# Kernel tuning notes

Hardware: AMD Instinct MI355X
Metric: run time of the kernel (lower is better)

## Reference

```python
import jax, jax.numpy as jnp
import numpy as np

N_NODES = 100_000
N_EDGES = 3_200_000
NUM_FEATURES = 128
EMB = 128
GNN_LAYERS = 3
N_GRAPHS = 512
FILL = 2.0  # improved=True -> self-loop weight 2


def setup_inputs() -> dict:
    key = jax.random.key(0)
    ks = jax.random.split(key, 8)
    x = jax.random.normal(ks[0], (N_NODES, NUM_FEATURES), jnp.float32)
    edge_index = jax.random.randint(ks[1], (2, N_EDGES), 0, N_NODES, dtype=jnp.int64)
    batch_index = jnp.sort(jax.random.randint(ks[2], (N_NODES,), 0, N_GRAPHS, dtype=jnp.int64))
    W0 = jax.random.normal(ks[3], (NUM_FEATURES, EMB), jnp.float32) / np.float32(np.sqrt(NUM_FEATURES))
    b0 = jnp.zeros((EMB,), jnp.float32)
    W_hid = jax.random.normal(ks[4], (GNN_LAYERS - 1, EMB, EMB), jnp.float32) / np.float32(np.sqrt(EMB))
    b_hid = jnp.zeros((GNN_LAYERS - 1, EMB), jnp.float32)
    W_out = jax.random.normal(ks[5], (2 * EMB, 1), jnp.float32) / np.float32(np.sqrt(2 * EMB))
    b_out = jnp.zeros((1,), jnp.float32)
    return {"x": x, "edge_index": edge_index, "batch_index": batch_index,
            "W0": W0, "b0": b0, "W_hid": W_hid, "b_hid": b_hid,
            "W_out": W_out, "b_out": b_out}


def _gcn_norm(edge_index, n_nodes):
    # add self-loops (weight=FILL for improved=True), symmetric D^-1/2 A D^-1/2 norm
    loop = jnp.arange(n_nodes)
    row = jnp.concatenate([edge_index[0], loop])
    col = jnp.concatenate([edge_index[1], loop])
    w = jnp.concatenate([jnp.ones((edge_index.shape[1],), jnp.float32),
                         jnp.full((n_nodes,), FILL, jnp.float32)])
    deg = jax.ops.segment_sum(w, col, num_segments=n_nodes)
    dinv = jnp.where(deg > 0, jax.lax.rsqrt(deg), 0.0)
    return row, col, dinv[row] * w * dinv[col]


def _gcn_conv(h, W, b, row, col, norm, n_nodes):
    h = h @ W                              # [N, emb]
    msg = h[row] * norm[:, None]           # gather + scale over edges
    return jax.ops.segment_sum(msg, col, num_segments=n_nodes) + b


def reference(x, edge_index, batch_index, W0, b0, W_hid, b_hid, W_out, b_out):
    n = x.shape[0]
    row, col, norm = _gcn_norm(edge_index, n)
    h = jnp.tanh(_gcn_conv(x, W0, b0, row, col, norm, n))
    for i in range(W_hid.shape[0]):
        h = jnp.tanh(_gcn_conv(h, W_hid[i], b_hid[i], row, col, norm, n))
    cnt = jax.ops.segment_sum(jnp.ones((n,), h.dtype), batch_index, num_segments=N_GRAPHS)
    mx = jax.ops.segment_max(h, batch_index, num_segments=N_GRAPHS)
    mx = jnp.where(cnt[:, None] > 0, mx, 0.0)            # gmp
    mean = jax.ops.segment_sum(h, batch_index, num_segments=N_GRAPHS) / jnp.maximum(cnt, 1.0)[:, None]  # gap
    pooled = jnp.concatenate([mx, mean], axis=1)          # [G, 2*emb]
    return pooled @ W_out + b_out                         # [G, 1]
```

## Files before the change

### kernel.cpp

```cpp
#include <hip/hip_runtime.h>
#include <math.h>

#define NF 128
#define SCAN_CHUNK 1024
#define BUCK_SHIFT 9
#define BUCK_CAP 20480
#define NBUCK_MAX 256
#define ECHUNK 2048

typedef int      vint4   __attribute__((ext_vector_type(4)));
typedef float    vfloat4 __attribute__((ext_vector_type(4)));
typedef float    f32x4   __attribute__((ext_vector_type(4)));
typedef _Float16 vhalf4  __attribute__((ext_vector_type(4)));
typedef _Float16 vhalf8  __attribute__((ext_vector_type(8)));

__global__ __launch_bounds__(256) void k_bucket(const int* __restrict__ row,
                                                const int* __restrict__ col,
                                                int* __restrict__ gcur,
                                                int* __restrict__ bdata, int E) {
  __shared__ int bcnt[NBUCK_MAX];
  __shared__ int bstage[NBUCK_MAX][32];
  const int tid = threadIdx.x;
  const int nChunks = (E + ECHUNK - 1) / ECHUNK;

  for (int chunk = blockIdx.x; chunk < nChunks; chunk += gridDim.x) {
    bcnt[tid] = 0;
    __syncthreads();

    const int cbase = chunk * ECHUNK;
    if (cbase + ECHUNK <= E) {
      const vint4* r4 = reinterpret_cast<const vint4*>(row) + (cbase >> 2) + 2 * tid;
      const vint4* c4 = reinterpret_cast<const vint4*>(col) + (cbase >> 2) + 2 * tid;
      vint4 ra = __builtin_nontemporal_load(&r4[0]);
      vint4 rb = __builtin_nontemporal_load(&r4[1]);
      vint4 ca = __builtin_nontemporal_load(&c4[0]);
      vint4 cb = __builtin_nontemporal_load(&c4[1]);
      int rr[8] = {ra.x, ra.y, ra.z, ra.w, rb.x, rb.y, rb.z, rb.w};
      int cc[8] = {ca.x, ca.y, ca.z, ca.w, cb.x, cb.y, cb.z, cb.w};
#pragma unroll
      for (int j = 0; j < 8; ++j) {
        int b = cc[j] >> BUCK_SHIFT;
        int packed = ((cc[j] & ((1 << BUCK_SHIFT) - 1)) << 17) | rr[j];
        int pos = atomicAdd(&bcnt[b], 1);
        if (pos < 32) {
          bstage[b][pos] = packed;
        } else {
          int p = atomicAdd(&gcur[b], 1);
          if (p < BUCK_CAP) bdata[b * BUCK_CAP + p] = packed;
        }
      }
    } else {
      for (int j = 0; j < 8; ++j) {
        int e = cbase + tid + j * 256;
        if (e < E) {
          int c = col[e], r = row[e];
          int b = c >> BUCK_SHIFT;
          int packed = ((c & ((1 << BUCK_SHIFT) - 1)) << 17) | r;
          int pos = atomicAdd(&bcnt[b], 1);
          if (pos < 32) {
            bstage[b][pos] = packed;
          } else {
            int p = atomicAdd(&gcur[b], 1);
            if (p < BUCK_CAP) bdata[b * BUCK_CAP + p] = packed;
          }
        }
      }
    }
    __syncthreads();

    int k = bcnt[tid];
    if (k > 32) k = 32;
    if (k > 0) {
      int p = atomicAdd(&gcur[tid], k);
      for (int i = 0; i < k && p + i < BUCK_CAP; ++i)
        bdata[tid * BUCK_CAP + p + i] = bstage[tid][i];
    }
    __syncthreads();
  }
}

__global__ __launch_bounds__(256) void k_hist(const int* __restrict__ gcur,
                                              const int* __restrict__ bdata,
                                              int* __restrict__ cnt, int N) {
  __shared__ int hist[1 << BUCK_SHIFT];
  const int b = blockIdx.x;
  const int tid = threadIdx.x;
  hist[tid] = 0;
  hist[tid + 256] = 0;
  __syncthreads();
  int nb = gcur[b];
  if (nb > BUCK_CAP) nb = BUCK_CAP;
  const int* bd = bdata + (size_t)b * BUCK_CAP;
  for (int i = tid; i < nb; i += 256) atomicAdd(&hist[bd[i] >> 17], 1);
  __syncthreads();
  int base = b << BUCK_SHIFT;
#pragma unroll
  for (int k = 0; k < (1 << BUCK_SHIFT); k += 256) {
    int node = base + k + tid;
    if (node < N) cnt[node] = hist[k + tid];
  }
}

__global__ __launch_bounds__(256) void k_scanA(const int* __restrict__ cnt,
                                               int* __restrict__ chunkTot, int N) {
  int c0 = blockIdx.x * SCAN_CHUNK + threadIdx.x * 4;
  int s = 0;
#pragma unroll
  for (int j = 0; j < 4; ++j) {
    int idx = c0 + j;
    if (idx < N) s += cnt[idx];
  }
  __shared__ int red[256];
  red[threadIdx.x] = s;
  __syncthreads();
  for (int o = 128; o > 0; o >>= 1) {
    if (threadIdx.x < o) red[threadIdx.x] += red[threadIdx.x + o];
    __syncthreads();
  }
  if (threadIdx.x == 0) chunkTot[blockIdx.x] = red[0];
}

__global__ __launch_bounds__(128) void k_scanB(const int* __restrict__ chunkTot,
                                               int* __restrict__ chunkOff, int nChunks) {
  __shared__ int buf[128];
  int t = threadIdx.x;
  int v = (t < nChunks) ? chunkTot[t] : 0;
  buf[t] = v;
  __syncthreads();
  for (int o = 1; o < 128; o <<= 1) {
    int x = buf[t];
    if (t >= o) x += buf[t - o];
    __syncthreads();
    buf[t] = x;
    __syncthreads();
  }
  if (t < nChunks) chunkOff[t] = buf[t] - v;
}

__global__ __launch_bounds__(256) void k_scanC(const int* __restrict__ cnt,
                                               const int* __restrict__ chunkOff,
                                               int* __restrict__ offs,
                                               float* __restrict__ dinv, int N) {
  int t = threadIdx.x;
  int c0 = blockIdx.x * SCAN_CHUNK + t * 4;
  int v[4];
  int s = 0;
#pragma unroll
  for (int j = 0; j < 4; ++j) {
    int idx = c0 + j;
    v[j] = (idx < N) ? cnt[idx] : 0;
    s += v[j];
  }
  __shared__ int buf[256];
  buf[t] = s;
  __syncthreads();
  for (int o = 1; o < 256; o <<= 1) {
    int x = buf[t];
    if (t >= o) x += buf[t - o];
    __syncthreads();
    buf[t] = x;
    __syncthreads();
  }
  int excl = buf[t] - s + chunkOff[blockIdx.x];
#pragma unroll
  for (int j = 0; j < 4; ++j) {
    int idx = c0 + j;
    if (idx < N) {
      offs[idx] = excl;
      dinv[idx] = rsqrtf((float)v[j] + 2.0f);
      excl += v[j];
    }
  }
}

__global__ __launch_bounds__(256) void k_bfill(const int* __restrict__ gcur,
                                               const int* __restrict__ bdata,
                                               const int* __restrict__ offs,
                                               int* __restrict__ csr, int N) {
  __shared__ int lcur[1 << BUCK_SHIFT];
  const int b = blockIdx.x;
  const int tid = threadIdx.x;
  const int base = b << BUCK_SHIFT;
#pragma unroll
  for (int k = 0; k < (1 << BUCK_SHIFT); k += 256) {
    int node = base + k + tid;
    lcur[k + tid] = (node < N) ? offs[node] : 0;
  }
  __syncthreads();
  int nb = gcur[b];
  if (nb > BUCK_CAP) nb = BUCK_CAP;
  const int* bd = bdata + (size_t)b * BUCK_CAP;
  for (int i = tid; i < nb; i += 256) {
    int v = bd[i];
    int p = atomicAdd(&lcur[v >> 17], 1);
    csr[p] = v & 0x1FFFF;
  }
}

__global__ __launch_bounds__(256) void k_wcvt(const float* __restrict__ W0,
                                              const float* __restrict__ Whid,
                                              _Float16* __restrict__ wt) {
  int g = blockIdx.x * 1024 + threadIdx.x * 4;
#pragma unroll
  for (int j = 0; j < 4; ++j) {
    int idx = g + j;
    int layer = idx >> 14;
    int within = idx & 16383;
    int c = within >> 7, k = within & 127;
    const float* src = (layer == 0) ? W0 : Whid + (layer - 1) * 16384;
    wt[idx] = (_Float16)src[k * 128 + c];
  }
}

template <bool F32IN>
__global__ __launch_bounds__(256) void k_gemm(const void* __restrict__ Hin,
                                              const _Float16* __restrict__ Wt,
                                              const float* __restrict__ dinv,
                                              _Float16* __restrict__ out, int nRows) {
  __shared__ _Float16 Wl[128][136];

  const int tid = threadIdx.x;
  for (int i = tid; i < 128 * 16; i += 256) {
    int r = i >> 4, seg = i & 15;
    *reinterpret_cast<vhalf8*>(&Wl[r][seg * 8]) =
        *reinterpret_cast<const vhalf8*>(Wt + r * 128 + seg * 8);
  }
  __syncthreads();

  const int l = tid & 63;
  const int wv = tid >> 6;
  const int lidx = l & 15;
  const int lk8 = (l >> 4) * 8;
  const int nodeBase = blockIdx.x * 128 + wv * 32;

  vhalf8 hfrag[2][4];
#pragma unroll
  for (int g = 0; g < 2; ++g) {
    int node = nodeBase + g * 16 + lidx;
    if (node < nRows) {
      if constexpr (F32IN) {
        const float* hp = (const float*)Hin + (size_t)node * NF + lk8;
#pragma unroll
        for (int kc = 0; kc < 4; ++kc) {
          vfloat4 lo = *reinterpret_cast<const vfloat4*>(hp + kc * 32);
          vfloat4 hi = *reinterpret_cast<const vfloat4*>(hp + kc * 32 + 4);
          vhalf8 v;
          v[0] = (_Float16)lo.x; v[1] = (_Float16)lo.y;
          v[2] = (_Float16)lo.z; v[3] = (_Float16)lo.w;
          v[4] = (_Float16)hi.x; v[5] = (_Float16)hi.y;
          v[6] = (_Float16)hi.z; v[7] = (_Float16)hi.w;
          hfrag[g][kc] = v;
        }
      } else {
        const _Float16* hp = (const _Float16*)Hin + (size_t)node * NF + lk8;
#pragma unroll
        for (int kc = 0; kc < 4; ++kc)
          hfrag[g][kc] = *reinterpret_cast<const vhalf8*>(hp + kc * 32);
      }
    } else {
#pragma unroll
      for (int kc = 0; kc < 4; ++kc)
#pragma unroll
        for (int j = 0; j < 8; ++j) hfrag[g][kc][j] = (_Float16)0.f;
    }
  }

  f32x4 acc[2][8];
#pragma unroll
  for (int g = 0; g < 2; ++g)
#pragma unroll
    for (int ct = 0; ct < 8; ++ct) acc[g][ct] = (f32x4)(0.f);

#pragma unroll
  for (int kc = 0; kc < 4; ++kc) {
#pragma unroll
    for (int ct = 0; ct < 8; ++ct) {
      vhalf8 w = *reinterpret_cast<const vhalf8*>(&Wl[ct * 16 + lidx][kc * 32 + lk8]);
      acc[0][ct] = __builtin_amdgcn_mfma_f32_16x16x32_f16(w, hfrag[0][kc], acc[0][ct], 0, 0, 0);
      acc[1][ct] = __builtin_amdgcn_mfma_f32_16x16x32_f16(w, hfrag[1][kc], acc[1][ct], 0, 0, 0);
    }
  }

  const int f0 = (l >> 4) * 4;
#pragma unroll
  for (int g = 0; g < 2; ++g) {
    int node = nodeBase + g * 16 + lidx;
    if (node < nRows) {
      float dv = dinv[node];
#pragma unroll
      for (int ct = 0; ct < 8; ++ct) {
        vhalf4 o;
        o.x = (_Float16)(dv * acc[g][ct][0]);
        o.y = (_Float16)(dv * acc[g][ct][1]);
        o.z = (_Float16)(dv * acc[g][ct][2]);
        o.w = (_Float16)(dv * acc[g][ct][3]);
        *reinterpret_cast<vhalf4*>(out + (size_t)node * NF + ct * 16 + f0) = o;
      }
    }
  }
}

__device__ __forceinline__ float4 h2f(vhalf4 v) {
  return make_float4((float)v.x, (float)v.y, (float)v.z, (float)v.w);
}
__device__ __forceinline__ float4 add4(float4 a, float4 acc) {
  acc.x += a.x; acc.y += a.y; acc.z += a.z; acc.w += a.w;
  return acc;
}

__global__ __launch_bounds__(256) void k_agg(const _Float16* __restrict__ tmp,
                                             const int* __restrict__ offs,
                                             const int* __restrict__ cnt,
                                             const int* __restrict__ csr,
                                             const float* __restrict__ dinv,
                                             const float* __restrict__ bias,
                                             _Float16* __restrict__ hout, int N) {
  int node = (blockIdx.x * 256 + threadIdx.x) >> 5;
  if (node >= N) return;
  int lane = threadIdx.x & 31;

  float dv = dinv[node];

  const vhalf4* t4 = reinterpret_cast<const vhalf4*>(tmp);
  float4 hv = h2f(t4[(size_t)node * 32 + lane]);
  float4 acc = make_float4(2.f * hv.x, 2.f * hv.y, 2.f * hv.z, 2.f * hv.w);

  int s = offs[node], e = s + cnt[node];
  int i = s;

  for (; (i & 3) && i < e; ++i) {
    float4 a = h2f(t4[(size_t)csr[i] * 32 + lane]);
    acc = add4(a, acc);
  }

  const vint4* cp = reinterpret_cast<const vint4*>(csr);
  for (; i + 8 <= e; i += 8) {
    vint4 p0 = __builtin_nontemporal_load(&cp[(i >> 2) + 0]);
    vint4 p1 = __builtin_nontemporal_load(&cp[(i >> 2) + 1]);
    float4 a0 = h2f(t4[(size_t)p0.x * 32 + lane]);
    float4 a1 = h2f(t4[(size_t)p0.y * 32 + lane]);
    float4 a2 = h2f(t4[(size_t)p0.z * 32 + lane]);
    float4 a3 = h2f(t4[(size_t)p0.w * 32 + lane]);
    float4 a4 = h2f(t4[(size_t)p1.x * 32 + lane]);
    float4 a5 = h2f(t4[(size_t)p1.y * 32 + lane]);
    float4 a6 = h2f(t4[(size_t)p1.z * 32 + lane]);
    float4 a7 = h2f(t4[(size_t)p1.w * 32 + lane]);
    acc = add4(a0, acc); acc = add4(a1, acc);
    acc = add4(a2, acc); acc = add4(a3, acc);
    acc = add4(a4, acc); acc = add4(a5, acc);
    acc = add4(a6, acc); acc = add4(a7, acc);
  }
  for (; i + 4 <= e; i += 4) {
    vint4 p = __builtin_nontemporal_load(&cp[i >> 2]);
    float4 a0 = h2f(t4[(size_t)p.x * 32 + lane]);
    float4 a1 = h2f(t4[(size_t)p.y * 32 + lane]);
    float4 a2 = h2f(t4[(size_t)p.z * 32 + lane]);
    float4 a3 = h2f(t4[(size_t)p.w * 32 + lane]);
    acc = add4(a0, acc); acc = add4(a1, acc);
    acc = add4(a2, acc); acc = add4(a3, acc);
  }
  for (; i < e; ++i) {
    float4 a = h2f(t4[(size_t)csr[i] * 32 + lane]);
    acc = add4(a, acc);
  }

  float4 b4 = reinterpret_cast<const float4*>(bias)[lane];
  vhalf4 r;
  r.x = (_Float16)tanhf(fmaf(dv, acc.x, b4.x));
  r.y = (_Float16)tanhf(fmaf(dv, acc.y, b4.y));
  r.z = (_Float16)tanhf(fmaf(dv, acc.z, b4.z));
  r.w = (_Float16)tanhf(fmaf(dv, acc.w, b4.w));
  __builtin_nontemporal_store(r, &reinterpret_cast<vhalf4*>(hout)[(size_t)node * 32 + lane]);
}

__global__ __launch_bounds__(512) void k_pool(const _Float16* __restrict__ h,
                                              const int* __restrict__ batch,
                                              const float* __restrict__ Wout,
                                              const float* __restrict__ bout,
                                              float* __restrict__ out, int N) {
  int g = blockIdx.x;

  int lo = 0, hi = N;
  while (lo < hi) { int mid = (lo + hi) >> 1; if (batch[mid] < g) lo = mid + 1; else hi = mid; }
  int s = lo;
  int lo2 = s, hi2 = N;
  while (lo2 < hi2) { int mid = (lo2 + hi2) >> 1; if (batch[mid] < g + 1) lo2 = mid + 1; else hi2 = mid; }
  int e = lo2;

  const int seg = threadIdx.x & 15;
  const int stripe = threadIdx.x >> 4;

  float mx[8], sm[8];
#pragma unroll
  for (int j = 0; j < 8; ++j) { mx[j] = -INFINITY; sm[j] = 0.f; }

  for (int n = s + stripe; n < e; n += 32) {
    vhalf8 v = *reinterpret_cast<const vhalf8*>(h + (size_t)n * NF + seg * 8);
#pragma unroll
    for (int j = 0; j < 8; ++j) {
      float f = (float)v[j];
      mx[j] = fmaxf(mx[j], f);
      sm[j] += f;
    }
  }

  __shared__ float smx[32][NF];
  __shared__ float ssm[32][NF];
#pragma unroll
  for (int j = 0; j < 8; ++j) {
    smx[stripe][seg * 8 + j] = mx[j];
    ssm[stripe][seg * 8 + j] = sm[j];
  }
  __syncthreads();

  for (int half = 16; half >= 1; half >>= 1) {
    if (stripe < half) {
#pragma unroll
      for (int j = 0; j < 8; ++j) {
        int f = seg * 8 + j;
        smx[stripe][f] = fmaxf(smx[stripe][f], smx[stripe + half][f]);
        ssm[stripe][f] += ssm[stripe + half][f];
      }
    }
    __syncthreads();
  }

  float part = 0.f;
  if (threadIdx.x < NF) {
    int f = threadIdx.x;
    float mxv = smx[0][f];
    float smv = ssm[0][f];
    int cntg = e - s;
    float mean = smv / fmaxf((float)cntg, 1.0f);
    if (cntg == 0) mxv = 0.f;
    part = mxv * Wout[f] + mean * Wout[NF + f];
  }
  for (int o = 32; o > 0; o >>= 1) part += __shfl_down(part, o);
  __shared__ float wsum[8];
  if ((threadIdx.x & 63) == 0) wsum[threadIdx.x >> 6] = part;
  __syncthreads();
  if (threadIdx.x == 0) out[g] = wsum[0] + wsum[1] + bout[0];
}

extern "C" void kernel_launch(void* const* d_in, const int* in_sizes, int n_in,
                              void* d_out, int out_size, void* d_ws, size_t ws_size,
                              hipStream_t stream) {
  const float* x     = (const float*)d_in[0];
  const int*   eidx  = (const int*)d_in[1];
  const int*   batch = (const int*)d_in[2];
  const float* W0    = (const float*)d_in[3];
  const float* b0    = (const float*)d_in[4];
  const float* Whid  = (const float*)d_in[5];
  const float* bhid  = (const float*)d_in[6];
  const float* Wout  = (const float*)d_in[7];
  const float* bout  = (const float*)d_in[8];
  float* out = (float*)d_out;

  const int N = in_sizes[0] / NF;
  const int E = in_sizes[1] / 2;
  const int G = out_size;

  const int* erow = eidx;
  const int* ecol = eidx + E;

  size_t off = 0;
  auto alloc = [&](size_t bytes) -> void* {
    void* p = (char*)d_ws + off;
    off += (bytes + 255) & ~(size_t)255;
    return p;
  };
  int*      gcur     = (int*)alloc(NBUCK_MAX * 4);
  int*      cnt      = (int*)alloc((size_t)N * 4);
  float*    dinv     = (float*)alloc((size_t)N * 4);
  int*      offs     = (int*)alloc((size_t)N * 4);
  int*      chunkTot = (int*)alloc(1024);
  int*      chunkOff = (int*)alloc(1024);
  int*      bdata    = (int*)alloc((size_t)NBUCK_MAX * BUCK_CAP * 4);
  int*      csr      = (int*)alloc((size_t)E * 4);
  _Float16* wt       = (_Float16*)alloc(3 * 16384 * 2);
  _Float16* tmp      = (_Float16*)alloc((size_t)N * NF * 2);
  _Float16* h        = (_Float16*)alloc((size_t)N * NF * 2);
  (void)ws_size;

  (void)hipMemsetAsync(gcur, 0, NBUCK_MAX * 4, stream);

  const int nChunks = (N + SCAN_CHUNK - 1) / SCAN_CHUNK;
  const int nbuck = (N + (1 << BUCK_SHIFT) - 1) >> BUCK_SHIFT;

  k_bucket<<<512, 256, 0, stream>>>(erow, ecol, gcur, bdata, E);
  k_hist<<<nbuck, 256, 0, stream>>>(gcur, bdata, cnt, N);
  k_scanA<<<nChunks, 256, 0, stream>>>(cnt, chunkTot, N);
  k_scanB<<<1, 128, 0, stream>>>(chunkTot, chunkOff, nChunks);
  k_scanC<<<nChunks, 256, 0, stream>>>(cnt, chunkOff, offs, dinv, N);
  k_bfill<<<nbuck, 256, 0, stream>>>(gcur, bdata, offs, csr, N);
  k_wcvt<<<48, 256, 0, stream>>>(W0, Whid, wt);

  const int gemmGrid = (N + 127) / 128;
  const int aggGrid = (N + 7) / 8;

  k_gemm<true><<<gemmGrid, 256, 0, stream>>>(x, wt, dinv, tmp, N);
  k_agg<<<aggGrid, 256, 0, stream>>>(tmp, offs, cnt, csr, dinv, b0, h, N);
  k_gemm<false><<<gemmGrid, 256, 0, stream>>>(h, wt + 16384, dinv, tmp, N);
  k_agg<<<aggGrid, 256, 0, stream>>>(tmp, offs, cnt, csr, dinv, bhid, h, N);
  k_gemm<false><<<gemmGrid, 256, 0, stream>>>(h, wt + 2 * 16384, dinv, tmp, N);
  k_agg<<<aggGrid, 256, 0, stream>>>(tmp, offs, cnt, csr, dinv, bhid + NF, h, N);

  k_pool<<<G, 512, 0, stream>>>(h, batch, Wout, bout, out, N);
}
```

Measured before the change: 520.1 us.

## Fuse histogram, scan and CSR fill into one per-bucket build kernel

Replaces the histogram, three-stage global prefix scan and bucket fill kernels with a single per-bucket kernel. Each bucket computes its own local histogram and scan, and writes CSR entries into a padded per-bucket region (offset b*BUCK_CAP), so no global scan is needed. This removes four kernel launches and a round trip of the count array through global memory. In exchange the CSR becomes sparse with gaps between buckets, using more memory and giving slightly less contiguous neighbour reads in aggregation.

```diff
diff --git a/kernel.cpp b/kernel.cpp
--- a/kernel.cpp
+++ b/kernel.cpp
@@ -2,7 +2,6 @@
 #include <math.h>
 
 #define NF 128
-#define SCAN_CHUNK 1024
 #define BUCK_SHIFT 9
 #define BUCK_CAP 20480
 #define NBUCK_MAX 256
@@ -79,117 +78,52 @@
   }
 }
 
-__global__ __launch_bounds__(256) void k_hist(const int* __restrict__ gcur,
-                                              const int* __restrict__ bdata,
-                                              int* __restrict__ cnt, int N) {
+__global__ __launch_bounds__(256) void k_build(const int* __restrict__ gcur,
+                                               const int* __restrict__ bdata,
+                                               int* __restrict__ csr,
+                                               int* __restrict__ offs,
+                                               int* __restrict__ cnt,
+                                               float* __restrict__ dinv, int N) {
   __shared__ int hist[1 << BUCK_SHIFT];
+  __shared__ int buf[256];
+  __shared__ int lcur[1 << BUCK_SHIFT];
   const int b = blockIdx.x;
   const int tid = threadIdx.x;
   hist[tid] = 0;
   hist[tid + 256] = 0;
   __syncthreads();
+
   int nb = gcur[b];
   if (nb > BUCK_CAP) nb = BUCK_CAP;
   const int* bd = bdata + (size_t)b * BUCK_CAP;
   for (int i = tid; i < nb; i += 256) atomicAdd(&hist[bd[i] >> 17], 1);
   __syncthreads();
-  int base = b << BUCK_SHIFT;
-#pragma unroll
-  for (int k = 0; k < (1 << BUCK_SHIFT); k += 256) {
-    int node = base + k + tid;
-    if (node < N) cnt[node] = hist[k + tid];
-  }
-}
-
-__global__ __launch_bounds__(256) void k_scanA(const int* __restrict__ cnt,
-                                               int* __restrict__ chunkTot, int N) {
-  int c0 = blockIdx.x * SCAN_CHUNK + threadIdx.x * 4;
-  int s = 0;
-#pragma unroll
-  for (int j = 0; j < 4; ++j) {
-    int idx = c0 + j;
-    if (idx < N) s += cnt[idx];
-  }
-  __shared__ int red[256];
-  red[threadIdx.x] = s;
-  __syncthreads();
-  for (int o = 128; o > 0; o >>= 1) {
-    if (threadIdx.x < o) red[threadIdx.x] += red[threadIdx.x + o];
-    __syncthreads();
-  }
-  if (threadIdx.x == 0) chunkTot[blockIdx.x] = red[0];
-}
-
-__global__ __launch_bounds__(128) void k_scanB(const int* __restrict__ chunkTot,
-                                               int* __restrict__ chunkOff, int nChunks) {
-  __shared__ int buf[128];
-  int t = threadIdx.x;
-  int v = (t < nChunks) ? chunkTot[t] : 0;
-  buf[t] = v;
-  __syncthreads();
-  for (int o = 1; o < 128; o <<= 1) {
-    int x = buf[t];
-    if (t >= o) x += buf[t - o];
-    __syncthreads();
-    buf[t] = x;
-    __syncthreads();
-  }
-  if (t < nChunks) chunkOff[t] = buf[t] - v;
-}
-
-__global__ __launch_bounds__(256) void k_scanC(const int* __restrict__ cnt,
-                                               const int* __restrict__ chunkOff,
-                                               int* __restrict__ offs,
-                                               float* __restrict__ dinv, int N) {
-  int t = threadIdx.x;
-  int c0 = blockIdx.x * SCAN_CHUNK + t * 4;
-  int v[4];
-  int s = 0;
-#pragma unroll
-  for (int j = 0; j < 4; ++j) {
-    int idx = c0 + j;
-    v[j] = (idx < N) ? cnt[idx] : 0;
-    s += v[j];
-  }
-  __shared__ int buf[256];
-  buf[t] = s;
+
+  int h0 = hist[2 * tid];
+  int h1 = hist[2 * tid + 1];
+  int s = h0 + h1;
+  buf[tid] = s;
   __syncthreads();
   for (int o = 1; o < 256; o <<= 1) {
-    int x = buf[t];
-    if (t >= o) x += buf[t - o];
-    __syncthreads();
-    buf[t] = x;
-    __syncthreads();
-  }
-  int excl = buf[t] - s + chunkOff[blockIdx.x];
-#pragma unroll
-  for (int j = 0; j < 4; ++j) {
-    int idx = c0 + j;
-    if (idx < N) {
-      offs[idx] = excl;
-      dinv[idx] = rsqrtf((float)v[j] + 2.0f);
-      excl += v[j];
-    }
-  }
-}
-
-__global__ __launch_bounds__(256) void k_bfill(const int* __restrict__ gcur,
-                                               const int* __restrict__ bdata,
-                                               const int* __restrict__ offs,
-                                               int* __restrict__ csr, int N) {
-  __shared__ int lcur[1 << BUCK_SHIFT];
-  const int b = blockIdx.x;
-  const int tid = threadIdx.x;
-  const int base = b << BUCK_SHIFT;
-#pragma unroll
-  for (int k = 0; k < (1 << BUCK_SHIFT); k += 256) {
-    int node = base + k + tid;
-    lcur[k + tid] = (node < N) ? offs[node] : 0;
-  }
-  __syncthreads();
-  int nb = gcur[b];
-  if (nb > BUCK_CAP) nb = BUCK_CAP;
-  const int* bd = bdata + (size_t)b * BUCK_CAP;
+    int x = buf[tid];
+    if (tid >= o) x += buf[tid - o];
+    __syncthreads();
+    buf[tid] = x;
+    __syncthreads();
+  }
+  int excl = buf[tid] - s;
+
+  const int nbase = b << BUCK_SHIFT;
+  const int cbase = b * BUCK_CAP;
+  int o0 = cbase + excl;
+  int o1 = o0 + h0;
+  lcur[2 * tid] = o0;
+  lcur[2 * tid + 1] = o1;
+  int n0 = nbase + 2 * tid, n1 = n0 + 1;
+  if (n0 < N) { offs[n0] = o0; cnt[n0] = h0; dinv[n0] = rsqrtf((float)h0 + 2.0f); }
+  if (n1 < N) { offs[n1] = o1; cnt[n1] = h1; dinv[n1] = rsqrtf((float)h1 + 2.0f); }
+  __syncthreads();
+
   for (int i = tid; i < nb; i += 256) {
     int v = bd[i];
     int p = atomicAdd(&lcur[v >> 17], 1);
@@ -473,10 +407,8 @@
   int*      cnt      = (int*)alloc((size_t)N * 4);
   float*    dinv     = (float*)alloc((size_t)N * 4);
   int*      offs     = (int*)alloc((size_t)N * 4);
-  int*      chunkTot = (int*)alloc(1024);
-  int*      chunkOff = (int*)alloc(1024);
   int*      bdata    = (int*)alloc((size_t)NBUCK_MAX * BUCK_CAP * 4);
-  int*      csr      = (int*)alloc((size_t)E * 4);
+  int*      csr      = (int*)alloc((size_t)NBUCK_MAX * BUCK_CAP * 4);
   _Float16* wt       = (_Float16*)alloc(3 * 16384 * 2);
   _Float16* tmp      = (_Float16*)alloc((size_t)N * NF * 2);
   _Float16* h        = (_Float16*)alloc((size_t)N * NF * 2);
@@ -484,15 +416,10 @@
 
   (void)hipMemsetAsync(gcur, 0, NBUCK_MAX * 4, stream);
 
-  const int nChunks = (N + SCAN_CHUNK - 1) / SCAN_CHUNK;
   const int nbuck = (N + (1 << BUCK_SHIFT) - 1) >> BUCK_SHIFT;
 
   k_bucket<<<512, 256, 0, stream>>>(erow, ecol, gcur, bdata, E);
-  k_hist<<<nbuck, 256, 0, stream>>>(gcur, bdata, cnt, N);
-  k_scanA<<<nChunks, 256, 0, stream>>>(cnt, chunkTot, N);
-  k_scanB<<<1, 128, 0, stream>>>(chunkTot, chunkOff, nChunks);
-  k_scanC<<<nChunks, 256, 0, stream>>>(cnt, chunkOff, offs, dinv, N);
-  k_bfill<<<nbuck, 256, 0, stream>>>(gcur, bdata, offs, csr, N);
+  k_build<<<nbuck, 256, 0, stream>>>(gcur, bdata, csr, offs, cnt, dinv, N);
   k_wcvt<<<48, 256, 0, stream>>>(W0, Whid, wt);
 
   const int gemmGrid = (N + 127) / 128;
```

After: 505.7 us. 1.03x faster.
